# Kernel optimization log

Measured on AMD Instinct MI355X. Metric: run time of the kernel, lower is better.

## Reference

```python
import jax, jax.numpy as jnp
import numpy as np

EMB_DIM = 1024
N_HEAD = 16
HEAD_DIM = EMB_DIM // N_HEAD  # 64
NUM_KV = 1
SEQ = 2048
BATCH = 2
QKV_OUT = (N_HEAD + 2 * NUM_KV) * HEAD_DIM  # 1152
ROPE_THETA = 10000.0


def _rope_tables(seq_len, dim):
    inv_freq = 1.0 / (ROPE_THETA ** (jnp.arange(0, dim, 2, dtype=jnp.float32) / dim))  # [dim/2]
    pos = jnp.arange(seq_len, dtype=jnp.float32)
    ang = pos[:, None] * inv_freq[None, :]  # [S, dim/2]
    return jnp.cos(ang), jnp.sin(ang)


def _apply_rope(x, cos, sin):
    # x: [B, S, H, D]; interleaved-pair rotation (torchtune-style)
    B, S, H, D = x.shape
    xr = x.reshape(B, S, H, D // 2, 2)
    x1, x2 = xr[..., 0], xr[..., 1]
    c = cos[None, :, None, :]
    s = sin[None, :, None, :]
    o1 = x1 * c - x2 * s
    o2 = x1 * s + x2 * c
    return jnp.stack([o1, o2], axis=-1).reshape(B, S, H, D)


def setup_inputs() -> dict:
    key = jax.random.key(0)
    k1, k2, k3, k4, k5 = jax.random.split(key, 5)
    scale = 1.0 / np.sqrt(EMB_DIM)
    return {
        "x": jax.random.normal(k1, (BATCH, SEQ, EMB_DIM), dtype=jnp.float32),
        "qkv_w": jax.random.uniform(k2, (QKV_OUT, EMB_DIM), jnp.float32, -scale, scale),
        "qkv_b": jax.random.uniform(k3, (QKV_OUT,), jnp.float32, -scale, scale),
        "out_w": jax.random.uniform(k4, (EMB_DIM, EMB_DIM), jnp.float32, -scale, scale),
        "out_b": jax.random.uniform(k5, (EMB_DIM,), jnp.float32, -scale, scale),
    }


def reference(x, qkv_w, qkv_b, out_w, out_b):
    B, S, E = x.shape
    qkv = x @ qkv_w.T + qkv_b  # [B, S, 1152]
    q_size = N_HEAD * HEAD_DIM
    kv_size = NUM_KV * HEAD_DIM
    q = qkv[..., :q_size].reshape(B, S, N_HEAD, HEAD_DIM)
    k = qkv[..., q_size:q_size + kv_size].reshape(B, S, NUM_KV, HEAD_DIM)
    v = qkv[..., q_size + kv_size:].reshape(B, S, NUM_KV, HEAD_DIM)

    cos, sin = _rope_tables(S, HEAD_DIM)
    q = _apply_rope(q, cos, sin)
    k = _apply_rope(k, cos, sin)

    q = q.transpose(0, 2, 1, 3)  # [B, H, S, D]
    k = k.transpose(0, 2, 1, 3)  # [B, 1, S, D]
    v = v.transpose(0, 2, 1, 3)  # [B, 1, S, D]

    # MQA: single KV head broadcasts over N_HEAD query heads
    scores = jnp.matmul(q, jnp.swapaxes(k, -2, -1)) / np.sqrt(HEAD_DIM)  # [B,H,S,S]
    causal = jnp.tril(jnp.ones((S, S), dtype=bool))
    scores = jnp.where(causal[None, None, :, :], scores, -jnp.inf)
    attn = jax.nn.softmax(scores, axis=-1)
    out = jnp.matmul(attn, v)  # [B, H, S, D]
    out = out.transpose(0, 2, 1, 3).reshape(B, S, E)
    return out @ out_w.T + out_b
```

## Files before the change

kernel.cpp:

```cpp
#include <hip/hip_runtime.h>
#include <stdint.h>
#include <stddef.h>

#define SEQ   2048
#define EMB   1024
#define NHEAD 16
#define HDIM  64
#define QKVO  1152
#define MTOT  4096

typedef __attribute__((ext_vector_type(4))) float f32x4;
typedef __attribute__((ext_vector_type(8))) short short8;
typedef __attribute__((ext_vector_type(4))) short s16x4;

__device__ __forceinline__ short f2bf(float f) {
  union { float f; unsigned u; } v; v.f = f;
  unsigned r = v.u + 0x7FFFu + ((v.u >> 16) & 1u);
  return (short)(r >> 16);
}

__device__ __forceinline__ unsigned cvtpk_bf16(float lo, float hi) {
  unsigned r;
  asm("v_cvt_pk_bf16_f32 %0, %1, %2" : "=v"(r) : "v"(lo), "v"(hi));
  return r;
}

__device__ __forceinline__ void gload16(const void* g, void* l) {
  __builtin_amdgcn_global_load_lds((const __attribute__((address_space(1))) void*)g,
                                   (__attribute__((address_space(3))) void*)l,
                                   16, 0, 0);
}

#define PX   524288
#define PW1  671744
#define PW2  802816
#define PTOT 811008

__device__ __forceinline__ void cvt8(const float* __restrict__ s, short* __restrict__ d) {
  float4 a = ((const float4*)s)[0];
  float4 b = ((const float4*)s)[1];
  short8 r;
  r[0]=f2bf(a.x); r[1]=f2bf(a.y); r[2]=f2bf(a.z); r[3]=f2bf(a.w);
  r[4]=f2bf(b.x); r[5]=f2bf(b.y); r[6]=f2bf(b.z); r[7]=f2bf(b.w);
  *(short8*)d = r;
}

__global__ __launch_bounds__(256) void prep_kernel(
    const float* __restrict__ x, const float* __restrict__ wqkv, const float* __restrict__ wout,
    short* __restrict__ xb, short* __restrict__ wqkvb, short* __restrict__ woutb,
    float* __restrict__ cost, float* __restrict__ sint) {
  int c = blockIdx.x * 256 + threadIdx.x;
  if (c < PX) {
    cvt8(x + (size_t)c * 8, xb + (size_t)c * 8);
  } else if (c < PW1) {
    int c2 = c - PX;
    cvt8(wqkv + (size_t)c2 * 8, wqkvb + (size_t)c2 * 8);
  } else if (c < PW2) {
    int c2 = c - PW1;
    cvt8(wout + (size_t)c2 * 8, woutb + (size_t)c2 * 8);
  } else if (c < PTOT) {
    int c2 = c - PW2;
    #pragma unroll
    for (int t = 0; t < 8; ++t) {
      int idx = c2 * 8 + t;
      int pos = idx >> 5, i = idx & 31;
      float inv = powf(10000.0f, -(float)i * (1.0f / 32.0f));
      float ang = (float)pos * inv;
      float sv, cv;
      sincosf(ang, &sv, &cv);
      cost[idx] = cv; sint[idx] = sv;
    }
  }
}

__device__ __forceinline__ void gemm_mainloop(
    const short* __restrict__ A, const short* __restrict__ Bm,
    int m0, int n0, short* ls, f32x4 acc[4][4]) {
  const int w = threadIdx.x >> 6, lane = threadIdx.x & 63;
  const int wm = w >> 1, wn = w & 1;
  const int lrow = lane & 15, lk = (lane >> 4) * 8;
  #pragma unroll
  for (int mi = 0; mi < 4; ++mi)
    #pragma unroll
    for (int ni = 0; ni < 4; ++ni)
      acc[mi][ni] = (f32x4){0.f, 0.f, 0.f, 0.f};

  const int srow8 = lane >> 3;
  const int scol = ((lane & 7) * 8) ^ (srow8 << 3);
  const int rswz = (lrow & 7) << 3;

  #define GSTAGE(buf, kt)                                                     \
    _Pragma("unroll")                                                         \
    for (int ii = 0; ii < 4; ++ii) {                                          \
      int seg = w * 4 + ii;                                                   \
      int row = seg * 8 + srow8;                                              \
      gload16(A  + (size_t)(m0 + row) * 1024 + (kt) + scol, (buf) + seg * 512);\
      gload16(Bm + (size_t)(n0 + row) * 1024 + (kt) + scol, (buf) + 8192 + seg * 512);\
    }

  GSTAGE(ls, 0);
  for (int t = 0; t < 16; ++t) {
    short* cur = ls + (t & 1) * 16384;
    short* nxt = ls + ((t + 1) & 1) * 16384;
    if (t < 15) {
      GSTAGE(nxt, (t + 1) * 64);
      asm volatile("s_waitcnt vmcnt(8)" ::: "memory");
    } else {
      asm volatile("s_waitcnt vmcnt(0)" ::: "memory");
    }
    __builtin_amdgcn_sched_barrier(0);
    __builtin_amdgcn_s_barrier();
    __builtin_amdgcn_sched_barrier(0);
    #pragma unroll
    for (int ks = 0; ks < 2; ++ks) {
      short8 af[4], bfv[4];
      #pragma unroll
      for (int mi = 0; mi < 4; ++mi)
        af[mi] = *(const short8*)(cur + (wm * 64 + mi * 16 + lrow) * 64 + ((lk + ks * 32) ^ rswz));
      #pragma unroll
      for (int ni = 0; ni < 4; ++ni)
        bfv[ni] = *(const short8*)(cur + 8192 + (wn * 64 + ni * 16 + lrow) * 64 + ((lk + ks * 32) ^ rswz));
      #pragma unroll
      for (int mi = 0; mi < 4; ++mi)
        #pragma unroll
        for (int ni = 0; ni < 4; ++ni)
          acc[mi][ni] = __builtin_amdgcn_mfma_f32_16x16x32_bf16(af[mi], bfv[ni], acc[mi][ni], 0, 0, 0);
    }
    __builtin_amdgcn_sched_barrier(0);
    __builtin_amdgcn_s_barrier();
  }
  #undef GSTAGE
}

#define QSCALE 0.180336880111124f

__global__ __launch_bounds__(256, 2) void qkv_kernel(
    const short* __restrict__ xb, const short* __restrict__ wb,
    const float* __restrict__ bias, const float* __restrict__ cost, const float* __restrict__ sint,
    short* __restrict__ qbuf, short* __restrict__ kbuf, short* __restrict__ vt) {
  __shared__ __align__(16) short ls[32768];
  f32x4 acc[4][4];
  const int m0 = blockIdx.x * 128, n0 = blockIdx.y * 128;
  gemm_mainloop(xb, wb, m0, n0, ls, acc);

  const int w = threadIdx.x >> 6, lane = threadIdx.x & 63;
  const int wm = w >> 1, wn = w & 1;
  const int colb = n0 + wn * 64 + (lane & 15);
  const int rowb = m0 + wm * 64 + ((lane >> 4) << 2);
  #pragma unroll
  for (int ni = 0; ni < 4; ++ni) {
    const int col = colb + ni * 16;
    const float bv = bias[col];
    #pragma unroll
    for (int mi = 0; mi < 4; ++mi) {
      #pragma unroll
      for (int j = 0; j < 4; ++j) {
        const int m = rowb + mi * 16 + j;
        const int bb = m >> 11, pos = m & 2047;
        float v = acc[mi][ni][j] + bv;
        float vp = __shfl_xor(v, 1);
        float ov;
        if (col < 1088) {
          const int d = (col < 1024) ? (col & 63) : (col - 1024);
          const int i = d >> 1;
          const float cv = cost[pos * 32 + i], sv = sint[pos * 32 + i];
          ov = ((col & 1) == 0) ? (v * cv - vp * sv)
                                : (vp * sv + v * cv);
          if (col < 1024) ov *= QSCALE;
        } else {
          ov = v;
        }
        const short bfo = f2bf(ov);
        if (col < 1024) {
          const int h = col >> 6;
          qbuf[(((size_t)bb * NHEAD + h) * SEQ + pos) * HDIM + (col & 63)] = bfo;
        } else if (col < 1088) {
          kbuf[((size_t)bb * SEQ + pos) * HDIM + (col - 1024)] = bfo;
        } else {
          vt[((size_t)bb * HDIM + (col - 1088)) * SEQ + pos] = bfo;
        }
      }
    }
  }
}

template<bool MASKED>
__device__ __forceinline__ void attn_tile(
    const short* __restrict__ Kb, const short* __restrict__ Vb,
    int kv0, int qg, int g, int sadr0, int sadr1, int pswz,
    short* pls,
    short8 qf0, short8 qf1, float& m_run, float& l_run, f32x4 o[4]) {
  f32x4 st[4];
  __builtin_amdgcn_s_setprio(1);
  #pragma unroll
  for (int r = 0; r < 4; ++r) {
    short8 k0 = *(const short8*)(Kb + sadr0 + r * 1024);
    short8 k1 = *(const short8*)(Kb + sadr1 + r * 1024);
    f32x4 z = (f32x4){0.f, 0.f, 0.f, 0.f};
    z = __builtin_amdgcn_mfma_f32_16x16x32_bf16(k0, qf0, z, 0, 0, 0);
    z = __builtin_amdgcn_mfma_f32_16x16x32_bf16(k1, qf1, z, 0, 0, 0);
    st[r] = z;
  }
  __builtin_amdgcn_s_setprio(0);
  float s[16];
  #pragma unroll
  for (int r = 0; r < 4; ++r)
    #pragma unroll
    for (int j = 0; j < 4; ++j) {
      if (MASKED) {
        const int kv = kv0 + r * 16 + g * 4 + j;
        s[r * 4 + j] = (kv <= qg) ? st[r][j] : -1.0e38f;
      } else {
        s[r * 4 + j] = st[r][j];
      }
    }
  float a0 = fmaxf(fmaxf(s[0], s[1]), s[2]);
  float a1 = fmaxf(fmaxf(s[3], s[4]), s[5]);
  float a2 = fmaxf(fmaxf(s[6], s[7]), s[8]);
  float a3 = fmaxf(fmaxf(s[9], s[10]), s[11]);
  float a4 = fmaxf(fmaxf(s[12], s[13]), s[14]);
  float b0 = fmaxf(fmaxf(a0, a1), a2);
  float b1 = fmaxf(fmaxf(a3, a4), s[15]);
  float mt = fmaxf(b0, b1);
  mt = fmaxf(mt, __shfl_xor(mt, 16));
  mt = fmaxf(mt, __shfl_xor(mt, 32));
  if (!__all(mt <= m_run + 11.0f)) {
    const float m_new = fmaxf(m_run, mt);
    const float sc = __builtin_amdgcn_exp2f(m_run - m_new);
    #pragma unroll
    for (int nf = 0; nf < 4; ++nf) o[nf] *= sc;
    l_run *= sc;
    m_run = m_new;
  }
  float p[16], ps = 0.f;
  #pragma unroll
  for (int i = 0; i < 16; ++i) { p[i] = __builtin_amdgcn_exp2f(s[i] - m_run); ps += p[i]; }
  ps += __shfl_xor(ps, 16);
  ps += __shfl_xor(ps, 32);
  l_run += ps;
  #pragma unroll
  for (int r = 0; r < 4; ++r)
    #pragma unroll
    for (int jj = 0; jj < 4; jj += 2) {
      unsigned pk = cvtpk_bf16(p[r * 4 + jj], p[r * 4 + jj + 1]);
      *(unsigned*)(pls + ((r * 16 + g * 4 + jj) ^ pswz)) = pk;
    }
  short8 pb0 = *(const short8*)(pls + ((g * 8) ^ pswz));
  short8 pb1 = *(const short8*)(pls + ((32 + g * 8) ^ pswz));
  __builtin_amdgcn_s_setprio(1);
  #pragma unroll
  for (int nf = 0; nf < 4; ++nf) {
    short8 v0 = *(const short8*)(Vb + sadr0 + nf * 1024);
    short8 v1 = *(const short8*)(Vb + sadr1 + nf * 1024);
    o[nf] = __builtin_amdgcn_mfma_f32_16x16x32_bf16(v0, pb0, o[nf], 0, 0, 0);
    o[nf] = __builtin_amdgcn_mfma_f32_16x16x32_bf16(v1, pb1, o[nf], 0, 0, 0);
  }
  __builtin_amdgcn_s_setprio(0);
}

__device__ __forceinline__ void stage_kv(
    const short* __restrict__ kb_b, const short* __restrict__ vt_b, int kv0,
    short* Kb, short* Vb, int tid) {
  #pragma unroll
  for (int rd = 0; rd < 2; ++rd) {
    const int ci = rd * 256 + tid;
    const int r = ci >> 3;
    const int cs = ((ci & 7) * 8) ^ ((r & 7) << 3);
    gload16(kb_b + (size_t)(kv0 + r) * HDIM + cs, Kb + ci * 8);
  }
  #pragma unroll
  for (int rd = 0; rd < 2; ++rd) {
    const int ci = rd * 256 + tid;
    const int r = ci >> 3;
    const int cs = ((ci & 7) * 8) ^ ((r & 7) << 3);
    gload16(vt_b + (size_t)r * SEQ + kv0 + cs, Vb + ci * 8);
  }
}

__global__ __launch_bounds__(256, 4) void attn_kernel(
    const short* __restrict__ qb, const short* __restrict__ kb,
    const short* __restrict__ vt, short* __restrict__ ao) {
  __shared__ __align__(16) short Kls[2][4096];
  __shared__ __align__(16) short Vls[2][4096];
  __shared__ __align__(16) short plds[4][16][64];
  const int tid = threadIdx.x, w = tid >> 6, lane = tid & 63;
  const int bh = blockIdx.x, bb = bh >> 4, h = bh & 15;
  const int yy = blockIdx.y, kk = yy >> 3, bq = yy & 7;
  const int qchunk = (kk == 0) ? bq : (kk == 1) ? (15 - bq)
                   : (kk == 2) ? (16 + bq) : (31 - bq);
  const int q0 = qchunk * 64 + w * 16;
  const int g = lane >> 4, qloc = lane & 15;
  const int qg = q0 + qloc;

  const short* kb_b = kb + (size_t)bb * SEQ * HDIM;
  const short* vt_b = vt + (size_t)bb * HDIM * SEQ;

  const short* qbase = qb + (((size_t)bb * NHEAD + h) * SEQ + q0 + qloc) * HDIM + g * 8;
  short8 qf0 = *(const short8*)qbase;
  short8 qf1 = *(const short8*)(qbase + 32);

  f32x4 o[4];
  #pragma unroll
  for (int nf = 0; nf < 4; ++nf) o[nf] = (f32x4){0.f, 0.f, 0.f, 0.f};
  float m_run = -1.0e38f, l_run = 0.0f;

  short* pls = &plds[w][qloc][0];
  const int pswz = (qloc & 7) << 3;
  const int swm = (qloc & 7) << 3;
  const int sadr0 = qloc * 64 + ((g * 8) ^ swm);
  const int sadr1 = qloc * 64 + ((g * 8 + 32) ^ swm);

  stage_kv(kb_b, vt_b, 0, Kls[0], Vls[0], tid);
  const int nt = qchunk + 1;
  for (int t = 0; t < nt; ++t) {
    if (t + 1 < nt) {
      stage_kv(kb_b, vt_b, (t + 1) * 64, Kls[(t + 1) & 1], Vls[(t + 1) & 1], tid);
      asm volatile("s_waitcnt vmcnt(4)" ::: "memory");
    } else {
      asm volatile("s_waitcnt vmcnt(0)" ::: "memory");
    }
    __builtin_amdgcn_sched_barrier(0);
    __builtin_amdgcn_s_barrier();
    __builtin_amdgcn_sched_barrier(0);
    const short* Kb = Kls[t & 1];
    const short* Vb = Vls[t & 1];
    if (t + 1 < nt)
      attn_tile<false>(Kb, Vb, t * 64, qg, g, sadr0, sadr1, pswz, pls, qf0, qf1, m_run, l_run, o);
    else
      attn_tile<true>(Kb, Vb, t * 64, qg, g, sadr0, sadr1, pswz, pls, qf0, qf1, m_run, l_run, o);
    __builtin_amdgcn_sched_barrier(0);
    __builtin_amdgcn_s_barrier();
  }

  const float inv = 1.0f / l_run;
  const size_t obase = ((size_t)bb * SEQ + q0 + qloc) * EMB + (size_t)h * HDIM + g * 4;
  #pragma unroll
  for (int nf = 0; nf < 4; ++nf) {
    s16x4 pk;
    #pragma unroll
    for (int j = 0; j < 4; ++j) pk[j] = f2bf(o[nf][j] * inv);
    *(s16x4*)(ao + obase + nf * 16) = pk;
  }
}

__global__ __launch_bounds__(256, 2) void out_kernel(
    const short* __restrict__ ab, const short* __restrict__ wb,
    const float* __restrict__ bias, float* __restrict__ out) {
  __shared__ __align__(16) short ls[32768];
  f32x4 acc[4][4];
  const int m0 = blockIdx.x * 128, n0 = blockIdx.y * 128;
  gemm_mainloop(ab, wb, m0, n0, ls, acc);

  const int w = threadIdx.x >> 6, lane = threadIdx.x & 63;
  const int wm = w >> 1, wn = w & 1;
  const int colb = n0 + wn * 64 + (lane & 15);
  const int rowb = m0 + wm * 64 + ((lane >> 4) << 2);
  #pragma unroll
  for (int ni = 0; ni < 4; ++ni) {
    const int col = colb + ni * 16;
    const float bv = bias[col];
    #pragma unroll
    for (int mi = 0; mi < 4; ++mi)
      #pragma unroll
      for (int j = 0; j < 4; ++j) {
        const int m = rowb + mi * 16 + j;
        out[(size_t)m * EMB + col] = acc[mi][ni][j] + bv;
      }
  }
}

extern "C" void kernel_launch(void* const* d_in, const int* in_sizes, int n_in,
                              void* d_out, int out_size, void* d_ws, size_t ws_size,
                              hipStream_t stream) {
  const float* x    = (const float*)d_in[0];
  const float* qkvw = (const float*)d_in[1];
  const float* qkvb = (const float*)d_in[2];
  const float* outw = (const float*)d_in[3];
  const float* outb = (const float*)d_in[4];
  float* out = (float*)d_out;
  char* ws = (char*)d_ws;

  short* xb    = (short*)(ws + 0);
  short* wqkvb = (short*)(ws + 8388608);
  short* woutb = (short*)(ws + 10747904);
  float* cost  = (float*)(ws + 12845056);
  float* sint  = (float*)(ws + 13107200);
  short* qbuf  = (short*)(ws + 13369344);
  short* kbuf  = (short*)(ws + 21757952);
  short* vtb   = (short*)(ws + 22282240);
  short* aob   = xb;

  prep_kernel<<<3168, 256, 0, stream>>>(x, qkvw, outw, xb, wqkvb, woutb, cost, sint);
  qkv_kernel<<<dim3(32, 9), 256, 0, stream>>>(xb, wqkvb, qkvb, cost, sint, qbuf, kbuf, vtb);
  attn_kernel<<<dim3(32, 32), 256, 0, stream>>>(qbuf, kbuf, vtb, aob);
  out_kernel<<<dim3(32, 8), 256, 0, stream>>>(aob, woutb, outb, out);
}
```

Before: 172.0 us.

## Shrink GEMM tiles to 64x64 with XCD-aware block remapping for QKV and output

Both projection GEMMs switch from 128x128 tiles to 64x64 tiles with half the LDS and a 4-per-CU occupancy hint, so the grids go from 288/256 workgroups to 1152/1024. The aim is to fill all CUs on the MI355X, since the old grids left many idle. A block-index swizzle groups neighbouring tiles onto the same XCD for L2 reuse. In exchange, each tile reuses less data per load, so global/L2 traffic and the share of LDS reads per MFMA both go up.

```diff
diff --git a/kernel.cpp b/kernel.cpp
--- a/kernel.cpp
+++ b/kernel.cpp
@@ -73,38 +73,39 @@
   }
 }
 
-__device__ __forceinline__ void gemm_mainloop(
+__device__ __forceinline__ void gstage64(
     const short* __restrict__ A, const short* __restrict__ Bm,
-    int m0, int n0, short* ls, f32x4 acc[4][4]) {
-  const int w = threadIdx.x >> 6, lane = threadIdx.x & 63;
+    int m0, int n0, int kt, short* buf, int tid) {
+  #pragma unroll
+  for (int rd = 0; rd < 2; ++rd) {
+    const int ci = rd * 256 + tid;
+    const int row = ci >> 3;
+    const int sc = ((ci & 7) * 8) ^ ((row & 7) << 3);
+    gload16(A  + (size_t)(m0 + row) * 1024 + kt + sc, buf + ci * 8);
+    gload16(Bm + (size_t)(n0 + row) * 1024 + kt + sc, buf + 4096 + ci * 8);
+  }
+}
+
+__device__ __forceinline__ void gemm_mainloop64(
+    const short* __restrict__ A, const short* __restrict__ Bm,
+    int m0, int n0, short* ls, f32x4 acc[2][2]) {
+  const int tid = threadIdx.x, w = tid >> 6, lane = tid & 63;
   const int wm = w >> 1, wn = w & 1;
   const int lrow = lane & 15, lk = (lane >> 4) * 8;
   #pragma unroll
-  for (int mi = 0; mi < 4; ++mi)
-    #pragma unroll
-    for (int ni = 0; ni < 4; ++ni)
+  for (int mi = 0; mi < 2; ++mi)
+    #pragma unroll
+    for (int ni = 0; ni < 2; ++ni)
       acc[mi][ni] = (f32x4){0.f, 0.f, 0.f, 0.f};
-
-  const int srow8 = lane >> 3;
-  const int scol = ((lane & 7) * 8) ^ (srow8 << 3);
   const int rswz = (lrow & 7) << 3;
 
-  #define GSTAGE(buf, kt)                                                     \
-    _Pragma("unroll")                                                         \
-    for (int ii = 0; ii < 4; ++ii) {                                          \
-      int seg = w * 4 + ii;                                                   \
-      int row = seg * 8 + srow8;                                              \
-      gload16(A  + (size_t)(m0 + row) * 1024 + (kt) + scol, (buf) + seg * 512);\
-      gload16(Bm + (size_t)(n0 + row) * 1024 + (kt) + scol, (buf) + 8192 + seg * 512);\
-    }
-
-  GSTAGE(ls, 0);
+  gstage64(A, Bm, m0, n0, 0, ls, tid);
   for (int t = 0; t < 16; ++t) {
-    short* cur = ls + (t & 1) * 16384;
-    short* nxt = ls + ((t + 1) & 1) * 16384;
+    short* cur = ls + (t & 1) * 8192;
+    short* nxt = ls + ((t + 1) & 1) * 8192;
     if (t < 15) {
-      GSTAGE(nxt, (t + 1) * 64);
-      asm volatile("s_waitcnt vmcnt(8)" ::: "memory");
+      gstage64(A, Bm, m0, n0, (t + 1) * 64, nxt, tid);
+      asm volatile("s_waitcnt vmcnt(4)" ::: "memory");
     } else {
       asm volatile("s_waitcnt vmcnt(0)" ::: "memory");
     }
@@ -113,46 +114,52 @@
     __builtin_amdgcn_sched_barrier(0);
     #pragma unroll
     for (int ks = 0; ks < 2; ++ks) {
-      short8 af[4], bfv[4];
+      short8 af[2], bfv[2];
       #pragma unroll
-      for (int mi = 0; mi < 4; ++mi)
-        af[mi] = *(const short8*)(cur + (wm * 64 + mi * 16 + lrow) * 64 + ((lk + ks * 32) ^ rswz));
+      for (int mi = 0; mi < 2; ++mi) {
+        const int row = wm * 32 + mi * 16 + lrow;
+        af[mi] = *(const short8*)(cur + row * 64 + ((lk + ks * 32) ^ rswz));
+      }
       #pragma unroll
-      for (int ni = 0; ni < 4; ++ni)
-        bfv[ni] = *(const short8*)(cur + 8192 + (wn * 64 + ni * 16 + lrow) * 64 + ((lk + ks * 32) ^ rswz));
+      for (int ni = 0; ni < 2; ++ni) {
+        const int row = wn * 32 + ni * 16 + lrow;
+        bfv[ni] = *(const short8*)(cur + 4096 + row * 64 + ((lk + ks * 32) ^ rswz));
+      }
       #pragma unroll
-      for (int mi = 0; mi < 4; ++mi)
+      for (int mi = 0; mi < 2; ++mi)
         #pragma unroll
-        for (int ni = 0; ni < 4; ++ni)
+        for (int ni = 0; ni < 2; ++ni)
           acc[mi][ni] = __builtin_amdgcn_mfma_f32_16x16x32_bf16(af[mi], bfv[ni], acc[mi][ni], 0, 0, 0);
     }
     __builtin_amdgcn_sched_barrier(0);
     __builtin_amdgcn_s_barrier();
   }
-  #undef GSTAGE
 }
 
 #define QSCALE 0.180336880111124f
-
-__global__ __launch_bounds__(256, 2) void qkv_kernel(
+#define QKV_NN 18
+
+__global__ __launch_bounds__(256, 4) void qkv_kernel(
     const short* __restrict__ xb, const short* __restrict__ wb,
     const float* __restrict__ bias, const float* __restrict__ cost, const float* __restrict__ sint,
     short* __restrict__ qbuf, short* __restrict__ kbuf, short* __restrict__ vt) {
-  __shared__ __align__(16) short ls[32768];
-  f32x4 acc[4][4];
-  const int m0 = blockIdx.x * 128, n0 = blockIdx.y * 128;
-  gemm_mainloop(xb, wb, m0, n0, ls, acc);
+  __shared__ __align__(16) short ls[16384];
+  f32x4 acc[2][2];
+  const int nwg = 64 * QKV_NN;
+  const int wg = (blockIdx.x & 7) * (nwg >> 3) + (blockIdx.x >> 3);
+  const int m0 = (wg / QKV_NN) * 64, n0 = (wg % QKV_NN) * 64;
+  gemm_mainloop64(xb, wb, m0, n0, ls, acc);
 
   const int w = threadIdx.x >> 6, lane = threadIdx.x & 63;
   const int wm = w >> 1, wn = w & 1;
-  const int colb = n0 + wn * 64 + (lane & 15);
-  const int rowb = m0 + wm * 64 + ((lane >> 4) << 2);
-  #pragma unroll
-  for (int ni = 0; ni < 4; ++ni) {
+  const int colb = n0 + wn * 32 + (lane & 15);
+  const int rowb = m0 + wm * 32 + ((lane >> 4) << 2);
+  #pragma unroll
+  for (int ni = 0; ni < 2; ++ni) {
     const int col = colb + ni * 16;
     const float bv = bias[col];
     #pragma unroll
-    for (int mi = 0; mi < 4; ++mi) {
+    for (int mi = 0; mi < 2; ++mi) {
       #pragma unroll
       for (int j = 0; j < 4; ++j) {
         const int m = rowb + mi * 16 + j;
@@ -343,24 +350,28 @@
   }
 }
 
-__global__ __launch_bounds__(256, 2) void out_kernel(
+#define OUT_NN 16
+
+__global__ __launch_bounds__(256, 4) void out_kernel(
     const short* __restrict__ ab, const short* __restrict__ wb,
     const float* __restrict__ bias, float* __restrict__ out) {
-  __shared__ __align__(16) short ls[32768];
-  f32x4 acc[4][4];
-  const int m0 = blockIdx.x * 128, n0 = blockIdx.y * 128;
-  gemm_mainloop(ab, wb, m0, n0, ls, acc);
+  __shared__ __align__(16) short ls[16384];
+  f32x4 acc[2][2];
+  const int nwg = 64 * OUT_NN;
+  const int wg = (blockIdx.x & 7) * (nwg >> 3) + (blockIdx.x >> 3);
+  const int m0 = (wg >> 4) * 64, n0 = (wg & 15) * 64;
+  gemm_mainloop64(ab, wb, m0, n0, ls, acc);
 
   const int w = threadIdx.x >> 6, lane = threadIdx.x & 63;
   const int wm = w >> 1, wn = w & 1;
-  const int colb = n0 + wn * 64 + (lane & 15);
-  const int rowb = m0 + wm * 64 + ((lane >> 4) << 2);
-  #pragma unroll
-  for (int ni = 0; ni < 4; ++ni) {
+  const int colb = n0 + wn * 32 + (lane & 15);
+  const int rowb = m0 + wm * 32 + ((lane >> 4) << 2);
+  #pragma unroll
+  for (int ni = 0; ni < 2; ++ni) {
     const int col = colb + ni * 16;
     const float bv = bias[col];
     #pragma unroll
-    for (int mi = 0; mi < 4; ++mi)
+    for (int mi = 0; mi < 2; ++mi)
       #pragma unroll
       for (int j = 0; j < 4; ++j) {
         const int m = rowb + mi * 16 + j;
@@ -391,7 +402,7 @@
   short* aob   = xb;
 
   prep_kernel<<<3168, 256, 0, stream>>>(x, qkvw, outw, xb, wqkvb, woutb, cost, sint);
-  qkv_kernel<<<dim3(32, 9), 256, 0, stream>>>(xb, wqkvb, qkvb, cost, sint, qbuf, kbuf, vtb);
+  qkv_kernel<<<1152, 256, 0, stream>>>(xb, wqkvb, qkvb, cost, sint, qbuf, kbuf, vtb);
   attn_kernel<<<dim3(32, 32), 256, 0, stream>>>(qbuf, kbuf, vtb, aob);
-  out_kernel<<<dim3(32, 8), 256, 0, stream>>>(aob, woutb, outb, out);
-}
+  out_kernel<<<1024, 256, 0, stream>>>(aob, woutb, outb, out);
+}
```

Result: faster. 160.1 us (-6.9%).
